# Optimization experiments

Measured on AMD Instinct MI355X. Metric: run time of the kernel, lower is better.

The kernel has to match this reference:

```python
import jax, jax.numpy as jnp
import numpy as np

EPS = 1e-8

def setup_inputs() -> dict:
    key = jax.random.key(0)
    k1, = jax.random.split(key, 1)
    B, C, H, W = 2, 128, 512, 512
    inputs = jax.random.normal(k1, (B, C, H, W), dtype=jnp.float32)
    shape = (1, C, 1, 1)
    return {
        "inputs": inputs,
        "gammaRow": jnp.ones(shape, jnp.float32),
        "betaRow": jnp.zeros(shape, jnp.float32),
        "gammaCol": jnp.ones(shape, jnp.float32),
        "betaCol": jnp.zeros(shape, jnp.float32),
        "gammaIns": jnp.zeros(shape, jnp.float32),
        "betaIns": jnp.zeros(shape, jnp.float32),
    }

def _norm(x, axis, gamma, beta):
    mean = jnp.mean(x, axis=axis, keepdims=True)
    var = jnp.mean(jnp.square(x - mean), axis=axis, keepdims=True)  # biased var
    return gamma * (x - mean) / (jnp.sqrt(var + EPS) + EPS) + beta

def reference(inputs, gammaRow, betaRow, gammaCol, betaCol, gammaIns, betaIns):
    # inputs: [B, C, H, W]
    normRow = _norm(inputs, 3, gammaRow, betaRow)        # over width
    normCol = _norm(inputs, 2, gammaCol, betaCol)        # over height
    normIns = _norm(inputs, (2, 3), gammaIns, betaIns)   # instance norm
    return jnp.concatenate([normIns, normRow, normCol], axis=1)  # [B, 3C, H, W]
```

## Files before the change

kernel.cpp:

```cpp
#include <hip/hip_runtime.h>
#include <math.h>

#define EPSF 1e-8f

constexpr int Wd = 512;
constexpr int Hd = 512;
constexpr int Cd = 128;
constexpr int Bd = 2;
constexpr int HW = Hd * Wd;
constexpr int NPLANE = Bd * Cd;
constexpr int NTHREADS = 1024;
constexpr int NWAVES = NTHREADS / 64;

typedef float f32x4 __attribute__((ext_vector_type(4)));

__device__ __forceinline__ void store_nt(float* p, float4 v) {
    __builtin_nontemporal_store(*(f32x4*)&v, (f32x4*)p);
}

__global__ __launch_bounds__(NTHREADS, 1)
void ircn_fused(const float* __restrict__ x,
                const float* __restrict__ gRow, const float* __restrict__ bRow,
                const float* __restrict__ gCol, const float* __restrict__ bCol,
                const float* __restrict__ gIns, const float* __restrict__ bIns,
                float* __restrict__ out)
{
    __shared__ float sPartS[NWAVES][Wd];
    __shared__ float sPartQ[NWAVES][Wd];
    __shared__ float rowA[Hd], rowB[Hd];
    __shared__ float colA[Wd], colB[Wd];
    __shared__ float sWaveS[NWAVES], sWaveQ[NWAVES];
    __shared__ float sInsA, sInsB;

    const int plane = blockIdx.x;
    const int tid   = threadIdx.x;
    const int wave  = tid >> 6;
    const int lane  = tid & 63;
    const int c     = plane & (Cd - 1);

    const float gr = gRow[c], br = bRow[c];
    const float gc = gCol[c], bc = bCol[c];
    const float gi = gIns[c], bi = bIns[c];

    const float* __restrict__ px = x + (size_t)plane * HW;

    float colS[8] = {0,0,0,0,0,0,0,0};
    float colQ[8] = {0,0,0,0,0,0,0,0};

    for (int r = wave; r < Hd; r += NWAVES) {
        const float4 a = *(const float4*)(px + (size_t)r * Wd + 4 * lane);
        const float4 d = *(const float4*)(px + (size_t)r * Wd + 256 + 4 * lane);
        float ax = a.x * a.x, ay = a.y * a.y, az = a.z * a.z, aw = a.w * a.w;
        float dx = d.x * d.x, dy = d.y * d.y, dz = d.z * d.z, dw = d.w * d.w;
        colS[0] += a.x; colS[1] += a.y; colS[2] += a.z; colS[3] += a.w;
        colS[4] += d.x; colS[5] += d.y; colS[6] += d.z; colS[7] += d.w;
        colQ[0] += ax;  colQ[1] += ay;  colQ[2] += az;  colQ[3] += aw;
        colQ[4] += dx;  colQ[5] += dy;  colQ[6] += dz;  colQ[7] += dw;

        float rs = (a.x + a.y) + (a.z + a.w) + (d.x + d.y) + (d.z + d.w);
        float rq = (ax + ay) + (az + aw) + (dx + dy) + (dz + dw);
        #pragma unroll
        for (int off = 32; off > 0; off >>= 1) {
            rs += __shfl_down(rs, off, 64);
            rq += __shfl_down(rq, off, 64);
        }
        if (lane == 0) {
            float m = rs * (1.0f / Wd);
            float v = fmaxf(rq * (1.0f / Wd) - m * m, 0.0f);
            float inv = 1.0f / (sqrtf(v + EPSF) + EPSF);
            float aa = gr * inv;
            rowA[r] = aa;
            rowB[r] = br - aa * m;
        }
    }

    #pragma unroll
    for (int k = 0; k < 4; k++) {
        sPartS[wave][4 * lane + k]       = colS[k];
        sPartQ[wave][4 * lane + k]       = colQ[k];
        sPartS[wave][256 + 4 * lane + k] = colS[4 + k];
        sPartQ[wave][256 + 4 * lane + k] = colQ[4 + k];
    }
    __syncthreads();

    float insS = 0.0f, insQ = 0.0f;
    if (tid < Wd) {
        float s = 0.0f, q = 0.0f;
        #pragma unroll
        for (int wv = 0; wv < NWAVES; wv++) { s += sPartS[wv][tid]; q += sPartQ[wv][tid]; }
        float m = s * (1.0f / Hd);
        float v = fmaxf(q * (1.0f / Hd) - m * m, 0.0f);
        float inv = 1.0f / (sqrtf(v + EPSF) + EPSF);
        float aa = gc * inv;
        colA[tid] = aa;
        colB[tid] = bc - aa * m;
        insS = s; insQ = q;
    }
    #pragma unroll
    for (int off = 32; off > 0; off >>= 1) {
        insS += __shfl_down(insS, off, 64);
        insQ += __shfl_down(insQ, off, 64);
    }
    if (lane == 0) { sWaveS[wave] = insS; sWaveQ[wave] = insQ; }
    __syncthreads();
    if (tid == 0) {
        float S = 0.0f, Q = 0.0f;
        #pragma unroll
        for (int wv = 0; wv < NWAVES; wv++) { S += sWaveS[wv]; Q += sWaveQ[wv]; }
        float m = S * (1.0f / HW);
        float v = fmaxf(Q * (1.0f / HW) - m * m, 0.0f);
        float inv = 1.0f / (sqrtf(v + EPSF) + EPSF);
        float aa = gi * inv;
        sInsA = aa;
        sInsB = bi - aa * m;
    }
    __syncthreads();

    const float aI = sInsA, bI = sInsB;
    const size_t baseIns = ((size_t)((plane >> 7) * 3 * Cd + c)) << 18;
    float* __restrict__ outIns = out + baseIns;
    float* __restrict__ outRow = out + baseIns + ((size_t)Cd << 18);
    float* __restrict__ outCol = out + baseIns + ((size_t)(2 * Cd) << 18);

    constexpr int NITER = HW / 4 / NTHREADS;
    #pragma unroll 2
    for (int it = 0; it < NITER; ++it) {
        const int i4 = it * NTHREADS + tid;
        const int h  = i4 >> 7;
        const int w4 = i4 & 127;
        const size_t off = (size_t)i4 * 4;

        const float4 xv = *(const float4*)(px + off);
        const float aR = rowA[h], bR = rowB[h];
        const float4 aC = *(const float4*)(colA + 4 * w4);
        const float4 bC = *(const float4*)(colB + 4 * w4);

        float4 oI, oR, oC;
        oI.x = fmaf(aI, xv.x, bI);   oI.y = fmaf(aI, xv.y, bI);
        oI.z = fmaf(aI, xv.z, bI);   oI.w = fmaf(aI, xv.w, bI);
        oR.x = fmaf(aR, xv.x, bR);   oR.y = fmaf(aR, xv.y, bR);
        oR.z = fmaf(aR, xv.z, bR);   oR.w = fmaf(aR, xv.w, bR);
        oC.x = fmaf(aC.x, xv.x, bC.x); oC.y = fmaf(aC.y, xv.y, bC.y);
        oC.z = fmaf(aC.z, xv.z, bC.z); oC.w = fmaf(aC.w, xv.w, bC.w);

        store_nt(outIns + off, oI);
        store_nt(outRow + off, oR);
        store_nt(outCol + off, oC);
    }
}

extern "C" void kernel_launch(void* const* d_in, const int* in_sizes, int n_in,
                              void* d_out, int out_size, void* d_ws, size_t ws_size,
                              hipStream_t stream) {
    const float* x    = (const float*)d_in[0];
    const float* gRow = (const float*)d_in[1];
    const float* bRow = (const float*)d_in[2];
    const float* gCol = (const float*)d_in[3];
    const float* bCol = (const float*)d_in[4];
    const float* gIns = (const float*)d_in[5];
    const float* bIns = (const float*)d_in[6];
    float* out = (float*)d_out;

    ircn_fused<<<NPLANE, NTHREADS, 0, stream>>>(x, gRow, bRow, gCol, bCol,
                                                gIns, bIns, out);
}
```

Before: 966.6 us.

## Split fused norm kernel into stats pass and chunked apply pass

The single per-plane kernel is split into two launches. A stats kernel (one 1024-thread block per plane) writes the row, column and instance scale and shift coefficients to workspace. An apply kernel then uses 8 row-chunks per plane with 256-thread blocks to spread the write-heavy phase across more blocks and raise occupancy. The cost is a second launch and a second read of the 256 MB input, since the original kept the plane's data likely in cache between phases.

```diff
diff --git a/kernel.cpp b/kernel.cpp
--- a/kernel.cpp
+++ b/kernel.cpp
@@ -9,8 +9,14 @@
 constexpr int Bd = 2;
 constexpr int HW = Hd * Wd;
 constexpr int NPLANE = Bd * Cd;
-constexpr int NTHREADS = 1024;
-constexpr int NWAVES = NTHREADS / 64;
+
+constexpr int STHREADS = 1024;
+constexpr int NWAVES = STHREADS / 64;
+
+constexpr int ATHREADS = 256;
+constexpr int CHUNKS = 8;
+constexpr int CROWS = Hd / CHUNKS;
+constexpr int AITER = CROWS * Wd / 4 / ATHREADS;
 
 typedef float f32x4 __attribute__((ext_vector_type(4)));
 
@@ -18,19 +24,18 @@
     __builtin_nontemporal_store(*(f32x4*)&v, (f32x4*)p);
 }
 
-__global__ __launch_bounds__(NTHREADS, 1)
-void ircn_fused(const float* __restrict__ x,
+__global__ __launch_bounds__(STHREADS, 1)
+void ircn_stats(const float* __restrict__ x,
                 const float* __restrict__ gRow, const float* __restrict__ bRow,
                 const float* __restrict__ gCol, const float* __restrict__ bCol,
                 const float* __restrict__ gIns, const float* __restrict__ bIns,
-                float* __restrict__ out)
+                float* __restrict__ wsRowA, float* __restrict__ wsRowB,
+                float* __restrict__ wsColA, float* __restrict__ wsColB,
+                float* __restrict__ wsIns)
 {
     __shared__ float sPartS[NWAVES][Wd];
     __shared__ float sPartQ[NWAVES][Wd];
-    __shared__ float rowA[Hd], rowB[Hd];
-    __shared__ float colA[Wd], colB[Wd];
     __shared__ float sWaveS[NWAVES], sWaveQ[NWAVES];
-    __shared__ float sInsA, sInsB;
 
     const int plane = blockIdx.x;
     const int tid   = threadIdx.x;
@@ -69,8 +74,8 @@
             float v = fmaxf(rq * (1.0f / Wd) - m * m, 0.0f);
             float inv = 1.0f / (sqrtf(v + EPSF) + EPSF);
             float aa = gr * inv;
-            rowA[r] = aa;
-            rowB[r] = br - aa * m;
+            wsRowA[plane * Hd + r] = aa;
+            wsRowB[plane * Hd + r] = br - aa * m;
         }
     }
 
@@ -92,8 +97,8 @@
         float v = fmaxf(q * (1.0f / Hd) - m * m, 0.0f);
         float inv = 1.0f / (sqrtf(v + EPSF) + EPSF);
         float aa = gc * inv;
-        colA[tid] = aa;
-        colB[tid] = bc - aa * m;
+        wsColA[plane * Wd + tid] = aa;
+        wsColB[plane * Wd + tid] = bc - aa * m;
         insS = s; insQ = q;
     }
     #pragma unroll
@@ -111,35 +116,58 @@
         float v = fmaxf(Q * (1.0f / HW) - m * m, 0.0f);
         float inv = 1.0f / (sqrtf(v + EPSF) + EPSF);
         float aa = gi * inv;
-        sInsA = aa;
-        sInsB = bi - aa * m;
-    }
+        wsIns[2 * plane]     = aa;
+        wsIns[2 * plane + 1] = bi - aa * m;
+    }
+}
+
+__global__ __launch_bounds__(ATHREADS, 4)
+void ircn_apply(const float* __restrict__ x,
+                const float* __restrict__ wsRowA, const float* __restrict__ wsRowB,
+                const float* __restrict__ wsColA, const float* __restrict__ wsColB,
+                const float* __restrict__ wsIns,
+                float* __restrict__ out)
+{
+    __shared__ float sRowA[CROWS], sRowB[CROWS];
+
+    const int tid   = threadIdx.x;
+    const int blk   = blockIdx.x;
+    const int plane = blk >> 3;
+    const int chunk = blk & (CHUNKS - 1);
+    const int c     = plane & (Cd - 1);
+    const int r0    = chunk * CROWS;
+
+    if (tid < CROWS) {
+        sRowA[tid] = wsRowA[plane * Hd + r0 + tid];
+        sRowB[tid] = wsRowB[plane * Hd + r0 + tid];
+    }
+    const int w4    = tid & 127;
+    const int hbase = tid >> 7;
+    const float4 aC = *(const float4*)(wsColA + plane * Wd + 4 * w4);
+    const float4 bC = *(const float4*)(wsColB + plane * Wd + 4 * w4);
+    const float  aI = wsIns[2 * plane];
+    const float  bI = wsIns[2 * plane + 1];
     __syncthreads();
 
-    const float aI = sInsA, bI = sInsB;
+    const size_t chunkOff = (size_t)r0 * Wd;
+    const float* __restrict__ px = x + (size_t)plane * HW + chunkOff;
     const size_t baseIns = ((size_t)((plane >> 7) * 3 * Cd + c)) << 18;
-    float* __restrict__ outIns = out + baseIns;
-    float* __restrict__ outRow = out + baseIns + ((size_t)Cd << 18);
-    float* __restrict__ outCol = out + baseIns + ((size_t)(2 * Cd) << 18);
-
-    constexpr int NITER = HW / 4 / NTHREADS;
+    float* __restrict__ outIns = out + baseIns + chunkOff;
+    float* __restrict__ outRow = outIns + ((size_t)Cd << 18);
+    float* __restrict__ outCol = outIns + ((size_t)(2 * Cd) << 18);
+
     #pragma unroll 2
-    for (int it = 0; it < NITER; ++it) {
-        const int i4 = it * NTHREADS + tid;
-        const int h  = i4 >> 7;
-        const int w4 = i4 & 127;
-        const size_t off = (size_t)i4 * 4;
-
+    for (int it = 0; it < AITER; ++it) {
+        const int h = 2 * it + hbase;
+        const size_t off = (size_t)h * Wd + 4 * w4;
         const float4 xv = *(const float4*)(px + off);
-        const float aR = rowA[h], bR = rowB[h];
-        const float4 aC = *(const float4*)(colA + 4 * w4);
-        const float4 bC = *(const float4*)(colB + 4 * w4);
+        const float aR = sRowA[h], bR = sRowB[h];
 
         float4 oI, oR, oC;
-        oI.x = fmaf(aI, xv.x, bI);   oI.y = fmaf(aI, xv.y, bI);
-        oI.z = fmaf(aI, xv.z, bI);   oI.w = fmaf(aI, xv.w, bI);
-        oR.x = fmaf(aR, xv.x, bR);   oR.y = fmaf(aR, xv.y, bR);
-        oR.z = fmaf(aR, xv.z, bR);   oR.w = fmaf(aR, xv.w, bR);
+        oI.x = fmaf(aI, xv.x, bI);     oI.y = fmaf(aI, xv.y, bI);
+        oI.z = fmaf(aI, xv.z, bI);     oI.w = fmaf(aI, xv.w, bI);
+        oR.x = fmaf(aR, xv.x, bR);     oR.y = fmaf(aR, xv.y, bR);
+        oR.z = fmaf(aR, xv.z, bR);     oR.w = fmaf(aR, xv.w, bR);
         oC.x = fmaf(aC.x, xv.x, bC.x); oC.y = fmaf(aC.y, xv.y, bC.y);
         oC.z = fmaf(aC.z, xv.z, bC.z); oC.w = fmaf(aC.w, xv.w, bC.w);
 
@@ -161,6 +189,16 @@
     const float* bIns = (const float*)d_in[6];
     float* out = (float*)d_out;
 
-    ircn_fused<<<NPLANE, NTHREADS, 0, stream>>>(x, gRow, bRow, gCol, bCol,
-                                                gIns, bIns, out);
-}
+    float* ws     = (float*)d_ws;
+    float* wsRowA = ws;
+    float* wsRowB = wsRowA + (size_t)NPLANE * Hd;
+    float* wsColA = wsRowB + (size_t)NPLANE * Hd;
+    float* wsColB = wsColA + (size_t)NPLANE * Wd;
+    float* wsIns  = wsColB + (size_t)NPLANE * Wd;
+
+    ircn_stats<<<NPLANE, STHREADS, 0, stream>>>(x, gRow, bRow, gCol, bCol,
+                                                gIns, bIns,
+                                                wsRowA, wsRowB, wsColA, wsColB, wsIns);
+    ircn_apply<<<NPLANE * CHUNKS, ATHREADS, 0, stream>>>(x, wsRowA, wsRowB,
+                                                         wsColA, wsColB, wsIns, out);
+}
```

Result: no change. 985.6 us (+2.0%).
